# Performance work log

Measured on AMD Instinct MI355X. Metric: run time of the kernel, lower is better.

Reference implementation:

```python
import jax, jax.numpy as jnp
import numpy as np

ALIGN_CORNERS = True   # module init arg
NUM_AUX = 8            # auxiliary samples for linearized multi-sampling
NOISE_STRENGTH = 0.5   # noise scale in units of input pixel spacing
EPS = 1e-6             # Tikhonov term for the per-pixel 2x2 least squares


def _base_coords(n, align_corners):
    if align_corners:
        return jnp.linspace(-1.0, 1.0, n, dtype=jnp.float32)
    return (jnp.arange(n, dtype=jnp.float32) * 2.0 + 1.0) / n - 1.0


def affine_grid(theta, h_out, w_out, align_corners):
    # theta: [B,2,3] -> grid [B,h_out,w_out,2] with (x,y) in [-1,1]
    xs = _base_coords(w_out, align_corners)
    ys = _base_coords(h_out, align_corners)
    X, Y = jnp.meshgrid(xs, ys)                      # [H,W]
    base = jnp.stack([X, Y, jnp.ones_like(X)], -1)   # [H,W,3]
    return jnp.einsum('hwk,bik->bhwi', base, theta)  # [B,H,W,2]


def bilinear_sample(image, grid, align_corners):
    # image [B,C,Hi,Wi], grid [B,H,W,2] -> [B,H,W,C], zero padding outside
    B, C, Hi, Wi = image.shape
    x, y = grid[..., 0], grid[..., 1]
    if align_corners:
        ix = (x + 1.0) * 0.5 * (Wi - 1)
        iy = (y + 1.0) * 0.5 * (Hi - 1)
    else:
        ix = ((x + 1.0) * Wi - 1.0) * 0.5
        iy = ((y + 1.0) * Hi - 1.0) * 0.5
    x0 = jnp.floor(ix); y0 = jnp.floor(iy)
    wx1 = ix - x0; wy1 = iy - y0
    bidx = jnp.arange(B)[:, None, None]

    def tap(xi, yi, w):
        valid = (xi >= 0) & (xi <= Wi - 1) & (yi >= 0) & (yi <= Hi - 1)
        xc = jnp.clip(xi, 0, Wi - 1).astype(jnp.int32)
        yc = jnp.clip(yi, 0, Hi - 1).astype(jnp.int32)
        v = image[bidx, :, yc, xc]                   # [B,H,W,C] gather
        return v * (w * valid)[..., None]

    return (tap(x0, y0, (1 - wx1) * (1 - wy1)) +
            tap(x0 + 1, y0, wx1 * (1 - wy1)) +
            tap(x0, y0 + 1, (1 - wx1) * wy1) +
            tap(x0 + 1, y0 + 1, wx1 * wy1))


def linearized_grid_sample(image, grid, align_corners):
    # Linearized multi-sampling (Jiang et al., ICCV'19): forward value equals
    # the center bilinear sample; gradient wrt grid flows through a per-pixel
    # least-squares linearization fitted from NUM_AUX noisy auxiliary samples.
    B, C, Hi, Wi = image.shape
    key = jax.random.key(42)
    spacing = jnp.array([2.0 / Wi, 2.0 / Hi], dtype=jnp.float32)  # one input pixel in norm coords
    g0 = jax.lax.stop_gradient(grid)
    noise = jax.random.normal(key, (B, NUM_AUX) + grid.shape[1:3] + (2,), dtype=jnp.float32)
    aux = g0[:, None] + noise * NOISE_STRENGTH * spacing          # [B,K,H,W,2]

    center = bilinear_sample(image, g0, align_corners)            # [B,H,W,C]
    samp = jax.vmap(lambda g: bilinear_sample(image, g, align_corners),
                    in_axes=1, out_axes=1)(aux)                   # [B,K,H,W,C]

    d_int = samp - center[:, None]                                # [B,K,H,W,C]
    d_grid = aux - g0[:, None]                                    # [B,K,H,W,2]
    xtx = jnp.einsum('bkhwi,bkhwj->bhwij', d_grid, d_grid) \
        + EPS * jnp.eye(2, dtype=jnp.float32)                     # [B,H,W,2,2]
    xty = jnp.einsum('bkhwi,bkhwc->bhwic', d_grid, d_int)         # [B,H,W,2,C]
    slope = jnp.linalg.solve(xtx, xty)                            # [B,H,W,2,C]

    out = center + jnp.einsum('bhwic,bhwi->bhwc', slope, grid - g0)
    return jnp.transpose(out, (0, 3, 1, 2))                       # [B,C,H,W]


def setup_inputs() -> dict:
    key = jax.random.key(0)
    k1, k2 = jax.random.split(key)
    B, C, Hi, Wi = 4, 3, 1024, 1024
    image = jax.random.normal(k1, (B, C, Hi, Wi), dtype=jnp.float32)
    ident = jnp.tile(jnp.array([[1.0, 0.0, 0.0], [0.0, 1.0, 0.0]], dtype=jnp.float32), (B, 1, 1))
    pMtrx = ident + 0.05 * jax.random.normal(k2, (B, 2, 3), dtype=jnp.float32)
    return {"image": image, "pMtrx": pMtrx, "W": 1024, "H": 1024}


def reference(image, pMtrx, W, H):
    # torch.affine_grid_generator(pMtrx, (B,3,W,H)) -> grid [B, W, H, 2]
    grid = affine_grid(pMtrx, W, H, ALIGN_CORNERS)
    return linearized_grid_sample(image, grid, ALIGN_CORNERS)  # [B,C,W,H]
```

## Files before the change

### kernel.cpp

```cpp
#include <hip/hip_runtime.h>


#define B_  4
#define C_  3
#define HI  1024
#define WI  1024
#define HO  1024
#define WO  1024

#define TW  32
#define TH  32
#define BANDW 52
#define BANDH 48
#define NSEG  13
#define SEGS_CH (BANDH * NSEG)
#define SEGS_TOT (C_ * SEGS_CH)
#define LDS_CH (BANDH * BANDW)
#define NITER ((SEGS_TOT + 63) / 64)

typedef __attribute__((address_space(3))) void* lds_vp;
typedef const __attribute__((address_space(1))) void* gbl_vp;

__device__ __forceinline__ float2 map_px(int w, int h,
                                         float t0, float t1, float t2,
                                         float t3, float t4, float t5) {
    const float xs = -1.0f + 2.0f * (float)w / (float)(WO - 1);
    const float ys = -1.0f + 2.0f * (float)h / (float)(HO - 1);
    const float x = t0 * xs + (t1 * ys + t2);
    const float y = t3 * xs + (t4 * ys + t5);
    const float ix = (x + 1.0f) * 0.5f * (float)(WI - 1);
    const float iy = (y + 1.0f) * 0.5f * (float)(HI - 1);
    return make_float2(ix, iy);
}

__global__ __launch_bounds__(256) void warp_bilinear_fast_kernel(
    const float* __restrict__ image,
    const float* __restrict__ theta,
    float* __restrict__ out)
{
    __shared__ float lds[NITER * 256];

    const int bid = blockIdx.x;
    const int b   = bid >> 10;
    const int rem = bid & 1023;
    const int h0  = (rem >> 5) * TH;
    const int w0  = (rem & 31) * TW;

    const float* t = theta + b * 6;
    const float t0 = t[0], t1 = t[1], t2 = t[2];
    const float t3 = t[3], t4 = t[4], t5 = t[5];

    const float2 c00 = map_px(w0,        h0,        t0,t1,t2,t3,t4,t5);
    const float2 c10 = map_px(w0+TW-1,   h0,        t0,t1,t2,t3,t4,t5);
    const float2 c01 = map_px(w0,        h0+TH-1,   t0,t1,t2,t3,t4,t5);
    const float2 c11 = map_px(w0+TW-1,   h0+TH-1,   t0,t1,t2,t3,t4,t5);

    const float ixmin = fminf(fminf(c00.x, c10.x), fminf(c01.x, c11.x));
    const float iymin = fminf(fminf(c00.y, c10.y), fminf(c01.y, c11.y));
    const float ixmax = fmaxf(fmaxf(c00.x, c10.x), fmaxf(c01.x, c11.x));
    const float iymax = fmaxf(fmaxf(c00.y, c10.y), fmaxf(c01.y, c11.y));

    int bx = (int)floorf(ixmin) - 1;
    bx = min(max(bx, 0), WI - BANDW);
    bx &= ~3;
    int by = (int)floorf(iymin) - 1;
    by = min(max(by, 0), HI - BANDH);

    const float* imgb = image + (size_t)b * (C_ * HI * WI);

    const int wv   = threadIdx.x >> 6;
    const int lane = threadIdx.x & 63;
#pragma unroll
    for (int j = wv; j < NITER; j += 4) {
        const int seg = j * 64 + lane;
        if (seg < SEGS_TOT) {
            const int c  = seg / SEGS_CH;
            const int r2 = seg - c * SEGS_CH;
            const int r  = r2 / NSEG;
            const int s  = r2 - r * NSEG;
            const float* gp = imgb + c * (HI * WI) + (by + r) * WI + (bx + s * 4);
            __builtin_amdgcn_global_load_lds((gbl_vp)gp, (lds_vp)(lds + j * 256),
                                             16, 0, 0);
        }
    }
    __syncthreads();

    const int wloc = threadIdx.x & 31;
    const int tyq  = threadIdx.x >> 5;
    const int w    = w0 + wloc;

    float* ob = out + (size_t)b * (C_ * HO * WO) + w;

    const bool interior = (ixmin >= 1.0f) && (ixmax <= (float)(WI - 2)) &&
                          (iymin >= 1.0f) && (iymax <= (float)(HI - 2));

    if (interior) {
#pragma unroll
        for (int k = 0; k < 4; ++k) {
            const int h = h0 + tyq + 8 * k;
            const float2 ixy = map_px(w, h, t0, t1, t2, t3, t4, t5);
            const float ix = ixy.x, iy = ixy.y;

            const float x0f = floorf(ix);
            const float y0f = floorf(iy);
            const float wx1 = ix - x0f;
            const float wy1 = iy - y0f;
            const float wx0 = 1.0f - wx1;
            const float wy0 = 1.0f - wy1;

            const float w00 = wx0 * wy0, w10 = wx1 * wy0;
            const float w01 = wx0 * wy1, w11 = wx1 * wy1;

            const int ox = (int)x0f - bx;
            const int oy = (int)y0f - by;
            const float* base0 = lds + oy * BANDW + ox;

#pragma unroll
            for (int c = 0; c < C_; ++c) {
                const float* p = base0 + c * LDS_CH;
                const float v = p[0]         * w00 + p[1]         * w10
                              + p[BANDW]     * w01 + p[BANDW + 1] * w11;
                __builtin_nontemporal_store(v, ob + c * (HO * WO) + h * WO);
            }
        }
    } else {
#pragma unroll
        for (int k = 0; k < 4; ++k) {
            const int h = h0 + tyq + 8 * k;
            const float2 ixy = map_px(w, h, t0, t1, t2, t3, t4, t5);
            const float ix = ixy.x, iy = ixy.y;

            const float x0f = floorf(ix);
            const float y0f = floorf(iy);
            const float wx1 = ix - x0f;
            const float wy1 = iy - y0f;
            const int x0 = (int)x0f;
            const int y0 = (int)y0f;

            const float ax0 = (1.0f - wx1) * ((x0 >= 0 && x0 <= WI - 1) ? 1.0f : 0.0f);
            const float ax1 = wx1          * ((x0 >= -1 && x0 <= WI - 2) ? 1.0f : 0.0f);
            const float ay0 = (1.0f - wy1) * ((y0 >= 0 && y0 <= HI - 1) ? 1.0f : 0.0f);
            const float ay1 = wy1          * ((y0 >= -1 && y0 <= HI - 2) ? 1.0f : 0.0f);

            const float w00 = ax0 * ay0, w10 = ax1 * ay0;
            const float w01 = ax0 * ay1, w11 = ax1 * ay1;

            const int xl0 = min(max(min(max(x0,     0), WI - 1) - bx, 0), BANDW - 1);
            const int xl1 = min(max(min(max(x0 + 1, 0), WI - 1) - bx, 0), BANDW - 1);
            const int yl0 = min(max(min(max(y0,     0), HI - 1) - by, 0), BANDH - 1);
            const int yl1 = min(max(min(max(y0 + 1, 0), HI - 1) - by, 0), BANDH - 1);

            const int o00 = yl0 * BANDW + xl0;
            const int o10 = yl0 * BANDW + xl1;
            const int o01 = yl1 * BANDW + xl0;
            const int o11 = yl1 * BANDW + xl1;

#pragma unroll
            for (int c = 0; c < C_; ++c) {
                const float* p = lds + c * LDS_CH;
                const float v = p[o00] * w00 + p[o10] * w10
                              + p[o01] * w01 + p[o11] * w11;
                __builtin_nontemporal_store(v, ob + c * (HO * WO) + h * WO);
            }
        }
    }
}

extern "C" void kernel_launch(void* const* d_in, const int* in_sizes, int n_in,
                              void* d_out, int out_size, void* d_ws, size_t ws_size,
                              hipStream_t stream) {
    const float* image = (const float*)d_in[0];
    const float* theta = (const float*)d_in[1];
    float* out = (float*)d_out;

    const int grid = B_ * (HO / TH) * (WO / TW);
    warp_bilinear_fast_kernel<<<grid, 256, 0, stream>>>(image, theta, out);
}
```

Before: 114.3 us.

## Size LDS staging band per tile from footprint and swizzle block order

Replaces the fixed 48x52 LDS band with a per-block band sized from the actual source footprint of the tile (rounded to 16-byte segments), so fewer global-to-LDS loads are issued. Divisions for segment indexing are replaced by float reciprocal multiplies. Block IDs are remapped to interleave across 8 groups, presumably to spread work across XCDs/L2 caches. This adds runtime index arithmetic and a dynamic loop bound, and the float-based division relies on exactness for small integers.

```diff
diff --git a/kernel.cpp b/kernel.cpp
--- a/kernel.cpp
+++ b/kernel.cpp
@@ -10,13 +10,8 @@
 
 #define TW  32
 #define TH  32
-#define BANDW 52
-#define BANDH 48
-#define NSEG  13
-#define SEGS_CH (BANDH * NSEG)
-#define SEGS_TOT (C_ * SEGS_CH)
-#define LDS_CH (BANDH * BANDW)
-#define NITER ((SEGS_TOT + 63) / 64)
+#define MAXSEG  13
+#define MAXROWS 48
 
 typedef __attribute__((address_space(3))) void* lds_vp;
 typedef const __attribute__((address_space(1))) void* gbl_vp;
@@ -38,11 +33,13 @@
     const float* __restrict__ theta,
     float* __restrict__ out)
 {
-    __shared__ float lds[NITER * 256];
+    __shared__ float lds[7680];
 
     const int bid = blockIdx.x;
-    const int b   = bid >> 10;
-    const int rem = bid & 1023;
+    const int sid = ((bid & 7) << 9) | (bid >> 3);
+
+    const int b   = sid >> 10;
+    const int rem = sid & 1023;
     const int h0  = (rem >> 5) * TH;
     const int w0  = (rem & 31) * TW;
 
@@ -60,26 +57,43 @@
     const float ixmax = fmaxf(fmaxf(c00.x, c10.x), fmaxf(c01.x, c11.x));
     const float iymax = fmaxf(fmaxf(c00.y, c10.y), fmaxf(c01.y, c11.y));
 
-    int bx = (int)floorf(ixmin) - 1;
-    bx = min(max(bx, 0), WI - BANDW);
-    bx &= ~3;
-    int by = (int)floorf(iymin) - 1;
-    by = min(max(by, 0), HI - BANDH);
+    int xlo = (int)floorf(ixmin) - 1;
+    int xhi = (int)floorf(ixmax) + 2;
+    xlo = min(max(xlo, 0), WI - 1);
+    xhi = min(max(xhi, xlo), WI - 1);
+    int bx = xlo & ~3;
+    const int nseg = min((xhi - bx + 4) >> 2, MAXSEG);
+    bx = min(bx, WI - 4 * nseg);
+
+    int ylo = (int)floorf(iymin) - 1;
+    int yhi = (int)floorf(iymax) + 2;
+    ylo = min(max(ylo, 0), HI - 1);
+    yhi = min(max(yhi, ylo), HI - 1);
+    const int nrows = min(yhi - ylo + 1, MAXROWS);
+    const int by = min(ylo, HI - nrows);
+
+    const int rowf   = nseg << 2;
+    const int segch  = nrows * nseg;
+    const int segtot = C_ * segch;
+    const int chf    = segch << 2;
+
+    const float rcp_segch = 1.0f / (float)segch;
+    const float rcp_nseg  = 1.0f / (float)nseg;
 
     const float* imgb = image + (size_t)b * (C_ * HI * WI);
 
     const int wv   = threadIdx.x >> 6;
     const int lane = threadIdx.x & 63;
-#pragma unroll
-    for (int j = wv; j < NITER; j += 4) {
-        const int seg = j * 64 + lane;
-        if (seg < SEGS_TOT) {
-            const int c  = seg / SEGS_CH;
-            const int r2 = seg - c * SEGS_CH;
-            const int r  = r2 / NSEG;
-            const int s  = r2 - r * NSEG;
-            const float* gp = imgb + c * (HI * WI) + (by + r) * WI + (bx + s * 4);
-            __builtin_amdgcn_global_load_lds((gbl_vp)gp, (lds_vp)(lds + j * 256),
+    const int niter = (segtot + 63) >> 6;
+    for (int j = wv; j < niter; j += 4) {
+        const int seg = (j << 6) + lane;
+        if (seg < segtot) {
+            const int c  = (int)(((float)seg + 0.5f) * rcp_segch);
+            const int r2 = seg - c * segch;
+            const int r  = (int)(((float)r2 + 0.5f) * rcp_nseg);
+            const int s  = r2 - r * nseg;
+            const float* gp = imgb + c * (HI * WI) + (by + r) * WI + (bx + (s << 2));
+            __builtin_amdgcn_global_load_lds((gbl_vp)gp, (lds_vp)(lds + (j << 8)),
                                              16, 0, 0);
         }
     }
@@ -113,13 +127,13 @@
 
             const int ox = (int)x0f - bx;
             const int oy = (int)y0f - by;
-            const float* base0 = lds + oy * BANDW + ox;
+            const float* base0 = lds + oy * rowf + ox;
 
 #pragma unroll
             for (int c = 0; c < C_; ++c) {
-                const float* p = base0 + c * LDS_CH;
-                const float v = p[0]         * w00 + p[1]         * w10
-                              + p[BANDW]     * w01 + p[BANDW + 1] * w11;
+                const float* p = base0 + c * chf;
+                const float v = p[0]        * w00 + p[1]        * w10
+                              + p[rowf]     * w01 + p[rowf + 1] * w11;
                 __builtin_nontemporal_store(v, ob + c * (HO * WO) + h * WO);
             }
         }
@@ -145,19 +159,20 @@
             const float w00 = ax0 * ay0, w10 = ax1 * ay0;
             const float w01 = ax0 * ay1, w11 = ax1 * ay1;
 
-            const int xl0 = min(max(min(max(x0,     0), WI - 1) - bx, 0), BANDW - 1);
-            const int xl1 = min(max(min(max(x0 + 1, 0), WI - 1) - bx, 0), BANDW - 1);
-            const int yl0 = min(max(min(max(y0,     0), HI - 1) - by, 0), BANDH - 1);
-            const int yl1 = min(max(min(max(y0 + 1, 0), HI - 1) - by, 0), BANDH - 1);
+            const int bw = (nseg << 2) - 1;
+            const int xl0 = min(max(min(max(x0,     0), WI - 1) - bx, 0), bw);
+            const int xl1 = min(max(min(max(x0 + 1, 0), WI - 1) - bx, 0), bw);
+            const int yl0 = min(max(min(max(y0,     0), HI - 1) - by, 0), nrows - 1);
+            const int yl1 = min(max(min(max(y0 + 1, 0), HI - 1) - by, 0), nrows - 1);
 
-            const int o00 = yl0 * BANDW + xl0;
-            const int o10 = yl0 * BANDW + xl1;
-            const int o01 = yl1 * BANDW + xl0;
-            const int o11 = yl1 * BANDW + xl1;
+            const int o00 = yl0 * rowf + xl0;
+            const int o10 = yl0 * rowf + xl1;
+            const int o01 = yl1 * rowf + xl0;
+            const int o11 = yl1 * rowf + xl1;
 
 #pragma unroll
             for (int c = 0; c < C_; ++c) {
-                const float* p = lds + c * LDS_CH;
+                const float* p = lds + c * chf;
                 const float v = p[o00] * w00 + p[o10] * w10
                               + p[o01] * w01 + p[o11] * w11;
                 __builtin_nontemporal_store(v, ob + c * (HO * WO) + h * WO);
```

After: 110.4 us. -3.5%, faster.

## Replace LDS band staging with direct global gathers and XCD-aware block swizzle

Applied to the files above, without the earlier changes.

Removes the per-block LDS staging of a 52x48 input band per channel and has each thread gather its four bilinear taps straight from global memory, relying on L2/cache reuse. Blocks now cover 64x4 output pixels with one pixel per thread, and block IDs are swizzled so consecutive blocks on the same XCD cover nearby tiles. This drops the LDS fill, barrier and redundant halo loads, in exchange for uncoalesced gather traffic through the cache hierarchy and more, smaller blocks.

```diff
diff --git a/kernel.cpp b/kernel.cpp
--- a/kernel.cpp
+++ b/kernel.cpp
@@ -8,18 +8,8 @@
 #define HO  1024
 #define WO  1024
 
-#define TW  32
-#define TH  32
-#define BANDW 52
-#define BANDH 48
-#define NSEG  13
-#define SEGS_CH (BANDH * NSEG)
-#define SEGS_TOT (C_ * SEGS_CH)
-#define LDS_CH (BANDH * BANDW)
-#define NITER ((SEGS_TOT + 63) / 64)
-
-typedef __attribute__((address_space(3))) void* lds_vp;
-typedef const __attribute__((address_space(1))) void* gbl_vp;
+#define BX  64
+#define BY  4
 
 __device__ __forceinline__ float2 map_px(int w, int h,
                                          float t0, float t1, float t2,
@@ -33,137 +23,116 @@
     return make_float2(ix, iy);
 }
 
-__global__ __launch_bounds__(256) void warp_bilinear_fast_kernel(
+__global__ __launch_bounds__(256) void warp_bilinear_direct_kernel(
     const float* __restrict__ image,
     const float* __restrict__ theta,
     float* __restrict__ out)
 {
-    __shared__ float lds[NITER * 256];
+    const int bid = blockIdx.x;
+    const int sid = ((bid & 7) << 11) | (bid >> 3);
 
-    const int bid = blockIdx.x;
-    const int b   = bid >> 10;
-    const int rem = bid & 1023;
-    const int h0  = (rem >> 5) * TH;
-    const int w0  = (rem & 31) * TW;
+    const int b   = sid >> 12;
+    const int rem = sid & 4095;
+    const int h0  = (rem >> 4) * BY;
+    const int w0  = (rem & 15) * BX;
 
     const float* t = theta + b * 6;
     const float t0 = t[0], t1 = t[1], t2 = t[2];
     const float t3 = t[3], t4 = t[4], t5 = t[5];
 
     const float2 c00 = map_px(w0,        h0,        t0,t1,t2,t3,t4,t5);
-    const float2 c10 = map_px(w0+TW-1,   h0,        t0,t1,t2,t3,t4,t5);
-    const float2 c01 = map_px(w0,        h0+TH-1,   t0,t1,t2,t3,t4,t5);
-    const float2 c11 = map_px(w0+TW-1,   h0+TH-1,   t0,t1,t2,t3,t4,t5);
+    const float2 c10 = map_px(w0+BX-1,   h0,        t0,t1,t2,t3,t4,t5);
+    const float2 c01 = map_px(w0,        h0+BY-1,   t0,t1,t2,t3,t4,t5);
+    const float2 c11 = map_px(w0+BX-1,   h0+BY-1,   t0,t1,t2,t3,t4,t5);
 
     const float ixmin = fminf(fminf(c00.x, c10.x), fminf(c01.x, c11.x));
     const float iymin = fminf(fminf(c00.y, c10.y), fminf(c01.y, c11.y));
     const float ixmax = fmaxf(fmaxf(c00.x, c10.x), fmaxf(c01.x, c11.x));
     const float iymax = fmaxf(fmaxf(c00.y, c10.y), fmaxf(c01.y, c11.y));
 
-    int bx = (int)floorf(ixmin) - 1;
-    bx = min(max(bx, 0), WI - BANDW);
-    bx &= ~3;
-    int by = (int)floorf(iymin) - 1;
-    by = min(max(by, 0), HI - BANDH);
-
-    const float* imgb = image + (size_t)b * (C_ * HI * WI);
-
-    const int wv   = threadIdx.x >> 6;
-    const int lane = threadIdx.x & 63;
-#pragma unroll
-    for (int j = wv; j < NITER; j += 4) {
-        const int seg = j * 64 + lane;
-        if (seg < SEGS_TOT) {
-            const int c  = seg / SEGS_CH;
-            const int r2 = seg - c * SEGS_CH;
-            const int r  = r2 / NSEG;
-            const int s  = r2 - r * NSEG;
-            const float* gp = imgb + c * (HI * WI) + (by + r) * WI + (bx + s * 4);
-            __builtin_amdgcn_global_load_lds((gbl_vp)gp, (lds_vp)(lds + j * 256),
-                                             16, 0, 0);
-        }
-    }
-    __syncthreads();
-
-    const int wloc = threadIdx.x & 31;
-    const int tyq  = threadIdx.x >> 5;
-    const int w    = w0 + wloc;
-
-    float* ob = out + (size_t)b * (C_ * HO * WO) + w;
-
     const bool interior = (ixmin >= 1.0f) && (ixmax <= (float)(WI - 2)) &&
                           (iymin >= 1.0f) && (iymax <= (float)(HI - 2));
 
+    const int tx = threadIdx.x & 63;
+    const int ty = threadIdx.x >> 6;
+    const int w  = w0 + tx;
+    const int h  = h0 + ty;
+
+    const float ys = -1.0f + 2.0f * (float)h / (float)(HO - 1);
+    const float xb = t1 * ys + t2;
+    const float yb = t4 * ys + t5;
+    const float xs = -1.0f + 2.0f * (float)w / (float)(WO - 1);
+    const float x  = t0 * xs + xb;
+    const float y  = t3 * xs + yb;
+    const float ix = (x + 1.0f) * 0.5f * (float)(WI - 1);
+    const float iy = (y + 1.0f) * 0.5f * (float)(HI - 1);
+
+    const float x0f = floorf(ix);
+    const float y0f = floorf(iy);
+    const float wx1 = ix - x0f;
+    const float wy1 = iy - y0f;
+
+    const float* imgb = image + (size_t)b * (C_ * HI * WI);
+    float* ob = out + (size_t)b * (C_ * HO * WO) + h * WO + w;
+
+    float v0, v1, v2;
+
     if (interior) {
-#pragma unroll
-        for (int k = 0; k < 4; ++k) {
-            const int h = h0 + tyq + 8 * k;
-            const float2 ixy = map_px(w, h, t0, t1, t2, t3, t4, t5);
-            const float ix = ixy.x, iy = ixy.y;
+        const float wx0 = 1.0f - wx1;
+        const float wy0 = 1.0f - wy1;
+        const float w00 = wx0 * wy0, w10 = wx1 * wy0;
+        const float w01 = wx0 * wy1, w11 = wx1 * wy1;
 
-            const float x0f = floorf(ix);
-            const float y0f = floorf(iy);
-            const float wx1 = ix - x0f;
-            const float wy1 = iy - y0f;
-            const float wx0 = 1.0f - wx1;
-            const float wy0 = 1.0f - wy1;
+        const int off = (int)y0f * WI + (int)x0f;
 
-            const float w00 = wx0 * wy0, w10 = wx1 * wy0;
-            const float w01 = wx0 * wy1, w11 = wx1 * wy1;
-
-            const int ox = (int)x0f - bx;
-            const int oy = (int)y0f - by;
-            const float* base0 = lds + oy * BANDW + ox;
-
-#pragma unroll
-            for (int c = 0; c < C_; ++c) {
-                const float* p = base0 + c * LDS_CH;
-                const float v = p[0]         * w00 + p[1]         * w10
-                              + p[BANDW]     * w01 + p[BANDW + 1] * w11;
-                __builtin_nontemporal_store(v, ob + c * (HO * WO) + h * WO);
-            }
+        {
+            const float* p = imgb + off;
+            v0 = p[0]  * w00 + p[1]      * w10
+               + p[WI] * w01 + p[WI + 1] * w11;
+        }
+        {
+            const float* p = imgb + (HI * WI) + off;
+            v1 = p[0]  * w00 + p[1]      * w10
+               + p[WI] * w01 + p[WI + 1] * w11;
+        }
+        {
+            const float* p = imgb + 2 * (HI * WI) + off;
+            v2 = p[0]  * w00 + p[1]      * w10
+               + p[WI] * w01 + p[WI + 1] * w11;
         }
     } else {
-#pragma unroll
-        for (int k = 0; k < 4; ++k) {
-            const int h = h0 + tyq + 8 * k;
-            const float2 ixy = map_px(w, h, t0, t1, t2, t3, t4, t5);
-            const float ix = ixy.x, iy = ixy.y;
+        const int x0 = (int)x0f;
+        const int y0 = (int)y0f;
 
-            const float x0f = floorf(ix);
-            const float y0f = floorf(iy);
-            const float wx1 = ix - x0f;
-            const float wy1 = iy - y0f;
-            const int x0 = (int)x0f;
-            const int y0 = (int)y0f;
+        const float ax0 = (1.0f - wx1) * ((x0 >= 0 && x0 <= WI - 1) ? 1.0f : 0.0f);
+        const float ax1 = wx1          * ((x0 >= -1 && x0 <= WI - 2) ? 1.0f : 0.0f);
+        const float ay0 = (1.0f - wy1) * ((y0 >= 0 && y0 <= HI - 1) ? 1.0f : 0.0f);
+        const float ay1 = wy1          * ((y0 >= -1 && y0 <= HI - 2) ? 1.0f : 0.0f);
 
-            const float ax0 = (1.0f - wx1) * ((x0 >= 0 && x0 <= WI - 1) ? 1.0f : 0.0f);
-            const float ax1 = wx1          * ((x0 >= -1 && x0 <= WI - 2) ? 1.0f : 0.0f);
-            const float ay0 = (1.0f - wy1) * ((y0 >= 0 && y0 <= HI - 1) ? 1.0f : 0.0f);
-            const float ay1 = wy1          * ((y0 >= -1 && y0 <= HI - 2) ? 1.0f : 0.0f);
+        const float w00 = ax0 * ay0, w10 = ax1 * ay0;
+        const float w01 = ax0 * ay1, w11 = ax1 * ay1;
 
-            const float w00 = ax0 * ay0, w10 = ax1 * ay0;
-            const float w01 = ax0 * ay1, w11 = ax1 * ay1;
+        const int xc0 = min(max(x0,     0), WI - 1);
+        const int xc1 = min(max(x0 + 1, 0), WI - 1);
+        const int yc0 = min(max(y0,     0), HI - 1);
+        const int yc1 = min(max(y0 + 1, 0), HI - 1);
 
-            const int xl0 = min(max(min(max(x0,     0), WI - 1) - bx, 0), BANDW - 1);
-            const int xl1 = min(max(min(max(x0 + 1, 0), WI - 1) - bx, 0), BANDW - 1);
-            const int yl0 = min(max(min(max(y0,     0), HI - 1) - by, 0), BANDH - 1);
-            const int yl1 = min(max(min(max(y0 + 1, 0), HI - 1) - by, 0), BANDH - 1);
+        const int o00 = yc0 * WI + xc0;
+        const int o10 = yc0 * WI + xc1;
+        const int o01 = yc1 * WI + xc0;
+        const int o11 = yc1 * WI + xc1;
 
-            const int o00 = yl0 * BANDW + xl0;
-            const int o10 = yl0 * BANDW + xl1;
-            const int o01 = yl1 * BANDW + xl0;
-            const int o11 = yl1 * BANDW + xl1;
+        v0 = imgb[o00] * w00 + imgb[o10] * w10
+           + imgb[o01] * w01 + imgb[o11] * w11;
+        v1 = imgb[HI*WI + o00] * w00 + imgb[HI*WI + o10] * w10
+           + imgb[HI*WI + o01] * w01 + imgb[HI*WI + o11] * w11;
+        v2 = imgb[2*HI*WI + o00] * w00 + imgb[2*HI*WI + o10] * w10
+           + imgb[2*HI*WI + o01] * w01 + imgb[2*HI*WI + o11] * w11;
+    }
 
-#pragma unroll
-            for (int c = 0; c < C_; ++c) {
-                const float* p = lds + c * LDS_CH;
-                const float v = p[o00] * w00 + p[o10] * w10
-                              + p[o01] * w01 + p[o11] * w11;
-                __builtin_nontemporal_store(v, ob + c * (HO * WO) + h * WO);
-            }
-        }
-    }
+    __builtin_nontemporal_store(v0, ob);
+    __builtin_nontemporal_store(v1, ob + (size_t)(HO * WO));
+    __builtin_nontemporal_store(v2, ob + (size_t)(2 * HO * WO));
 }
 
 extern "C" void kernel_launch(void* const* d_in, const int* in_sizes, int n_in,
@@ -173,6 +142,6 @@
     const float* theta = (const float*)d_in[1];
     float* out = (float*)d_out;
 
-    const int grid = B_ * (HO / TH) * (WO / TW);
-    warp_bilinear_fast_kernel<<<grid, 256, 0, stream>>>(image, theta, out);
+    const int grid = B_ * (HO / BY) * (WO / BX);
+    warp_bilinear_direct_kernel<<<grid, 256, 0, stream>>>(image, theta, out);
 }
```

Result: slower. 117.7 us (+2.9%).
